# Kernel tuning notes

Hardware: AMD Instinct MI355X
Metric: run time of the kernel (lower is better)

The kernel has to match this reference:

```python
import jax, jax.numpy as jnp
import numpy as np

H = W = 224
N_LM = 8
BLOCK = 3  # patch is [x-3:x+3, y-3:y+3] -> 6x6


def _clip_coords(lm_float):
    # lm_float: [B, 16] normalized landmarks in [0,1]
    c = (lm_float * 224.0).astype(jnp.int32)
    c = jnp.where(c >= 219, 200, c)
    c = jnp.where(c <= 5, 8, c)
    return c.reshape(c.shape[0], N_LM, 2)


def _gather_patches(pred_map, coords):
    # pred_map: [B,1,H,W], coords: [B,8,2] int32 -> [B,8,36]
    B = pred_map.shape[0]
    x = coords[..., 0]  # [B,8]
    y = coords[..., 1]
    offs = jnp.arange(-BLOCK, BLOCK)  # 6 offsets
    xs = x[..., None] + offs          # [B,8,6]
    ys = y[..., None] + offs          # [B,8,6]
    b = jnp.arange(B)[:, None, None, None]
    # vectorized gather replacing the per-sample/per-landmark python loop
    patches = pred_map[b, 0, xs[:, :, :, None], ys[:, :, None, :]]  # [B,8,6,6]
    return patches.reshape(B, N_LM, (2 * BLOCK) ** 2)


def setup_inputs() -> dict:
    key = jax.random.key(0)
    ks = jax.random.split(key, 8)
    B = 512
    pred_map = jax.random.normal(ks[0], (B, 1, H, W), dtype=jnp.float32)
    Landmarks_GT = jax.random.uniform(ks[1], (B, 16), dtype=jnp.float32)
    d_in = H * W  # 50176
    s1 = 1.0 / np.sqrt(d_in)
    s2 = 1.0 / np.sqrt(512)
    s3 = 1.0 / np.sqrt(256)
    W1 = jax.random.uniform(ks[2], (d_in, 512), jnp.float32, -s1, s1)
    b1 = jax.random.uniform(ks[3], (512,), jnp.float32, -s1, s1)
    W2 = jax.random.uniform(ks[4], (512, 256), jnp.float32, -s2, s2)
    b2 = jax.random.uniform(ks[5], (256,), jnp.float32, -s2, s2)
    W3 = jax.random.uniform(ks[6], (256, 16), jnp.float32, -s3, s3)
    b3 = jax.random.uniform(ks[7], (16,), jnp.float32, -s3, s3)
    return {"pred_map": pred_map, "Landmarks_GT": Landmarks_GT,
            "W1": W1, "b1": b1, "W2": W2, "b2": b2, "W3": W3, "b3": b3}


def reference(pred_map, Landmarks_GT, W1, b1, W2, b2, W3, b3):
    B = pred_map.shape[0]
    # GT landmark patch gather
    gt_coords = _clip_coords(Landmarks_GT)
    GT_patch = _gather_patches(pred_map, gt_coords)  # [B,8,36]
    # MLP_Grah_Second on flattened pred_map
    flat = pred_map.reshape(B, -1)                   # [B,50176]
    h = jax.nn.relu(flat @ W1 + b1)
    h = jax.nn.relu(h @ W2 + b2)
    pred = jax.nn.sigmoid(h @ W3 + b3)               # [B,16]
    # predicted landmark patch gather
    pr_coords = _clip_coords(pred)
    Pred_patch = _gather_patches(pred_map, pr_coords)  # [B,8,36]
    return pred, GT_patch, Pred_patch
```

## Files before the change

### kernel.cpp

```cpp
#include <hip/hip_runtime.h>
#include <math.h>

typedef __fp16   h16x2 __attribute__((ext_vector_type(2)));
typedef _Float16 f16x8 __attribute__((ext_vector_type(8)));
typedef __attribute__((ext_vector_type(4))) float f32x4;

#define KDIM 50176
#define NDIM 512
#define MDIM 512
#define BM 256
#define BN 128
#define BK 32

__device__ __forceinline__ void split_pair(float a, float b, unsigned& hw, unsigned& lw) {
    h16x2 hp = __builtin_amdgcn_cvt_pkrtz(a, b);
    float ra = (a - (float)hp[0]) * 2048.0f;
    float rb = (b - (float)hp[1]) * 2048.0f;
    h16x2 lp = __builtin_amdgcn_cvt_pkrtz(ra, rb);
    union { h16x2 v; unsigned u; } cu;
    cu.v = hp; hw = cu.u;
    cu.v = lp; lw = cu.u;
}

__global__ __launch_bounds__(512, 2) void gemm1_mfma(
    const float* __restrict__ A,
    const float* __restrict__ W,
    float* __restrict__ part,
    int steps, int S)
{
    __shared__ float          Afs[2][256][32];
    __shared__ unsigned short Bhs[2][128][40];
    __shared__ unsigned short Bls[2][128][40];

    const int t = threadIdx.x;

    const int nwg = 8 * S;
    int l = blockIdx.x;
    if ((nwg & 7) == 0) l = (l & 7) * (nwg >> 3) + (l >> 3);
    const int z = l >> 3, bm = l & 1, bn = (l >> 1) & 3;
    const int kbase = z * steps * BK;
    const int bmBase = bm * BM;

    const int lane = t & 63, wave = t >> 6;
    const int wm = wave >> 1, wn2 = wave & 1;
    const int l15 = lane & 15, lh = lane >> 4;

    const bool isW = (t < 256);
    const int u = isW ? t : (t - 256);
    const int wkb = u & 7, wn0 = (u >> 3) * 4;

    const int aRowInWave = lane >> 3;
    const int aSwz = ((lane & 7) ^ aRowInWave) * 4;

    f32x4 acc0[4][4], acc1[4][4];
#pragma unroll
    for (int i = 0; i < 4; ++i)
#pragma unroll
        for (int j = 0; j < 4; ++j) { acc0[i][j] = (f32x4)0.f; acc1[i][j] = (f32x4)0.f; }

    float4 wreg[4];
    auto gloadW = [&](int s) {
        const float* Wb = W + (size_t)(kbase + s * BK) * NDIM + bn * BN + wn0;
#pragma unroll
        for (int i = 0; i < 4; ++i)
            wreg[i] = *(const float4*)(Wb + (size_t)(wkb * 4 + i) * NDIM);
    };
    auto gloadA = [&](int s, int buf) {
        const int k0 = kbase + s * BK;
#pragma unroll
        for (int j = 0; j < 4; ++j) {
            const int rbase = wave * 32 + j * 8;
            const float* src = A + (size_t)(bmBase + rbase + aRowInWave) * KDIM + k0 + aSwz;
            __builtin_amdgcn_global_load_lds(src, &Afs[buf][rbase][0], 16, 0, 0);
        }
    };
    auto stageW = [&](int buf, int j) {
        unsigned h01, l01, h23, l23;
        split_pair(((const float*)&wreg[0])[j] * 64.0f, ((const float*)&wreg[1])[j] * 64.0f, h01, l01);
        split_pair(((const float*)&wreg[2])[j] * 64.0f, ((const float*)&wreg[3])[j] * 64.0f, h23, l23);
        *(uint2*)&Bhs[buf][wn0 + j][wkb * 4] = make_uint2(h01, h23);
        *(uint2*)&Bls[buf][wn0 + j][wkb * 4] = make_uint2(l01, l23);
    };

    auto buildA = [&](int buf, int mf, f16x8& ahv, f16x8& alv) {
        const int m = wm * 64 + mf * 16 + l15;
        const int s0 = ((2 * lh) ^ (l15 & 7)) * 4;
        const int s1 = ((2 * lh + 1) ^ (l15 & 7)) * 4;
        float4 f0 = *(const float4*)&Afs[buf][m][s0];
        float4 f1 = *(const float4*)&Afs[buf][m][s1];
        union { unsigned uu[4]; f16x8 v; } H, L;
        split_pair(f0.x, f0.y, H.uu[0], L.uu[0]);
        split_pair(f0.z, f0.w, H.uu[1], L.uu[1]);
        split_pair(f1.x, f1.y, H.uu[2], L.uu[2]);
        split_pair(f1.z, f1.w, H.uu[3], L.uu[3]);
        ahv = H.v; alv = L.v;
    };

    if (isW) gloadW(0);
    gloadA(0, 0);
    if (isW) {
#pragma unroll
        for (int j = 0; j < 4; ++j) stageW(0, j);
    }
    __syncthreads();

    int cur = 0;
    for (int s = 0; s < steps; ++s) {
        const bool pf = (s + 1 < steps);
        if (pf) {
            if (isW) gloadW(s + 1);
            gloadA(s + 1, cur ^ 1);
        }

        f16x8 bh[4], bl[4];
#pragma unroll
        for (int nf = 0; nf < 4; ++nf) {
            bh[nf] = *(const f16x8*)&Bhs[cur][wn2 * 64 + nf * 16 + l15][lh * 8];
            bl[nf] = *(const f16x8*)&Bls[cur][wn2 * 64 + nf * 16 + l15][lh * 8];
        }

        f16x8 ah[2], al[2];
        buildA(cur, 0, ah[0], al[0]);

#pragma unroll
        for (int mf = 0; mf < 4; ++mf) {
            const int c = mf & 1, n = c ^ 1;
            if (mf < 3) buildA(cur, mf + 1, ah[n], al[n]);
            __builtin_amdgcn_s_setprio(1);
#pragma unroll
            for (int nf = 0; nf < 4; ++nf) {
                acc0[mf][nf] = __builtin_amdgcn_mfma_f32_16x16x32_f16(ah[c], bh[nf], acc0[mf][nf], 0, 0, 0);
                acc1[mf][nf] = __builtin_amdgcn_mfma_f32_16x16x32_f16(ah[c], bl[nf], acc1[mf][nf], 0, 0, 0);
                acc1[mf][nf] = __builtin_amdgcn_mfma_f32_16x16x32_f16(al[c], bh[nf], acc1[mf][nf], 0, 0, 0);
            }
            __builtin_amdgcn_s_setprio(0);
            if (pf && isW) stageW(cur ^ 1, mf);
        }
        __syncthreads();
        cur ^= 1;
    }

    const float c0 = 1.0f / 64.0f;
    const float c1 = 1.0f / 131072.0f;
    float* Cp = part + (size_t)z * (MDIM * NDIM);
    const int row0 = bmBase + wm * 64;
    const int col0 = bn * BN + wn2 * 64;
#pragma unroll
    for (int mf = 0; mf < 4; ++mf)
#pragma unroll
        for (int nf = 0; nf < 4; ++nf) {
            const int r0 = row0 + mf * 16 + lh * 4;
            const int c = col0 + nf * 16 + l15;
#pragma unroll
            for (int r = 0; r < 4; ++r)
                Cp[(size_t)(r0 + r) * NDIM + c] = acc0[mf][nf][r] * c0 + acc1[mf][nf][r] * c1;
        }
}

__global__ __launch_bounds__(256) void reduce_bias_relu(
    const float4* __restrict__ part, const float* __restrict__ b1,
    float4* __restrict__ h1, int S)
{
    int i = blockIdx.x * 256 + threadIdx.x;
    float4 s = make_float4(0.f, 0.f, 0.f, 0.f);
    for (int z = 0; z < S; ++z) {
        float4 v = part[(size_t)z * 65536 + i];
        s.x += v.x; s.y += v.y; s.z += v.z; s.w += v.w;
    }
    int nb = (i & 127) * 4;
    s.x = fmaxf(s.x + b1[nb + 0], 0.f);
    s.y = fmaxf(s.y + b1[nb + 1], 0.f);
    s.z = fmaxf(s.z + b1[nb + 2], 0.f);
    s.w = fmaxf(s.w + b1[nb + 3], 0.f);
    h1[i] = s;
}

__global__ __launch_bounds__(256) void gemm2_k(
    const float* __restrict__ h1, const float* __restrict__ W2,
    const float* __restrict__ b2, float* __restrict__ h2)
{
    int g = blockIdx.x * 256 + threadIdx.x;
    int m = g >> 8, n = g & 255;
    const float* a = h1 + (size_t)m * 512;
    float sum = 0.f;
#pragma unroll 8
    for (int k = 0; k < 512; ++k) sum = fmaf(a[k], W2[(size_t)k * 256 + n], sum);
    sum += b2[n];
    h2[g] = fmaxf(sum, 0.f);
}

__global__ __launch_bounds__(256) void gemm3_sig(
    const float* __restrict__ h2, const float* __restrict__ W3,
    const float* __restrict__ b3, float* __restrict__ pred)
{
    int g = blockIdx.x * 256 + threadIdx.x;
    int m = g >> 4, j = g & 15;
    const float* a = h2 + (size_t)m * 256;
    float sum = 0.f;
#pragma unroll 8
    for (int k = 0; k < 256; ++k) sum = fmaf(a[k], W3[(size_t)k * 16 + j], sum);
    sum += b3[j];
    pred[g] = 1.f / (1.f + expf(-sum));
}

__device__ __forceinline__ int clip_coord(float v) {
    int c = (int)(v * 224.0f);
    if (c >= 219) c = 200;
    if (c <= 5)   c = 8;
    return c;
}

__global__ void patches_k(
    const float* __restrict__ pm, const float* __restrict__ gt,
    const float* __restrict__ pred, float* __restrict__ out)
{
    const int b = blockIdx.x;
    const int t = threadIdx.x;
    const int lm = t / 36, cell = t % 36;
    const int dx = cell / 6 - 3, dy = cell % 6 - 3;
    const float* pmb = pm + (size_t)b * 50176;
    {
        int cx = clip_coord(gt[b * 16 + lm * 2 + 0]);
        int cy = clip_coord(gt[b * 16 + lm * 2 + 1]);
        out[8192 + b * 288 + t] = pmb[(cx + dx) * 224 + (cy + dy)];
    }
    {
        int cx = clip_coord(pred[b * 16 + lm * 2 + 0]);
        int cy = clip_coord(pred[b * 16 + lm * 2 + 1]);
        out[8192 + 147456 + b * 288 + t] = pmb[(cx + dx) * 224 + (cy + dy)];
    }
}

extern "C" void kernel_launch(void* const* d_in, const int* in_sizes, int n_in,
                              void* d_out, int out_size, void* d_ws, size_t ws_size,
                              hipStream_t stream)
{
    const float* pred_map = (const float*)d_in[0];
    const float* gt       = (const float*)d_in[1];
    const float* W1       = (const float*)d_in[2];
    const float* b1       = (const float*)d_in[3];
    const float* W2       = (const float*)d_in[4];
    const float* b2       = (const float*)d_in[5];
    const float* W3       = (const float*)d_in[6];
    const float* b3       = (const float*)d_in[7];
    float* out = (float*)d_out;

    float* h1   = (float*)d_ws;
    float* h2   = h1 + 262144;
    float* part = h2 + 131072;

    static const int cand[] = {32, 16, 8, 4, 2, 1};
    int S = 1;
    for (int i = 0; i < 6; ++i) {
        size_t need = (size_t)(393216 + (size_t)cand[i] * 262144) * sizeof(float);
        if (need <= ws_size) { S = cand[i]; break; }
    }
    const int steps = 1568 / S;

    hipLaunchKernelGGL(gemm1_mfma, dim3(8 * S), dim3(512), 0, stream,
                       pred_map, W1, part, steps, S);
    hipLaunchKernelGGL(reduce_bias_relu, dim3(256), dim3(256), 0, stream,
                       (const float4*)part, b1, (float4*)h1, S);
    hipLaunchKernelGGL(gemm2_k, dim3(131072 / 256), dim3(256), 0, stream, h1, W2, b2, h2);
    hipLaunchKernelGGL(gemm3_sig, dim3(8192 / 256), dim3(256), 0, stream, h2, W3, b3, out);
    hipLaunchKernelGGL(patches_k, dim3(512), dim3(288), 0, stream, pred_map, gt, out, out);
}
```

Before: 159.0 us.

## Pre-split activations into fp16 hi/lo tiles in a separate pass before GEMM1

Adds a presplit kernel that converts pred_map once into swizzled fp16 high/low tile planes in workspace, and a new GEMM1 variant that loads these pre-split tiles straight into LDS. Before, each of the four N-column workgroups repeated the split for the same A tile. The change removes that redundant ALU work from the MFMA loop. In exchange it adds an extra pass that reads A and writes A-sized data, plus a workspace requirement; the old path stays as a fallback when workspace is too small.

After: 199.6 us. 25.6% more time.

```diff
diff --git a/kernel.cpp b/kernel.cpp
--- a/kernel.cpp
+++ b/kernel.cpp
@@ -3,7 +3,7 @@
 
 typedef __fp16   h16x2 __attribute__((ext_vector_type(2)));
 typedef _Float16 f16x8 __attribute__((ext_vector_type(8)));
-typedef __attribute__((ext_vector_type(4))) float f32x4;
+typedef __attribute__((ext_vector_type(4))) float    f32x4;
 
 #define KDIM 50176
 #define NDIM 512
@@ -11,6 +11,9 @@
 #define BM 256
 #define BN 128
 #define BK 32
+#define NSTEPS 1568
+#define TILE_HALFS 16384
+#define APL_FLOATS 25690112
 
 __device__ __forceinline__ void split_pair(float a, float b, unsigned& hw, unsigned& lw) {
     h16x2 hp = __builtin_amdgcn_cvt_pkrtz(a, b);
@@ -22,18 +25,162 @@
     cu.v = lp; lw = cu.u;
 }
 
-__global__ __launch_bounds__(512, 2) void gemm1_mfma(
-    const float* __restrict__ A,
+__global__ __launch_bounds__(256) void presplit_a(
+    const float* __restrict__ A, unsigned* __restrict__ Apl)
+{
+    const int NU = 2 * NSTEPS * 256 * 4;
+    for (int u = blockIdx.x * 256 + threadIdx.x; u < NU; u += gridDim.x * 256) {
+        const int kg = u & 3;
+        const int m  = (u >> 2) & 255;
+        const int ti = u >> 10;
+        const int s  = ti % NSTEPS;
+        const int bm = ti / NSTEPS;
+        const float* src = A + (size_t)(bm * 256 + m) * KDIM + s * BK + kg * 8;
+        float4 f0 = *(const float4*)(src);
+        float4 f1 = *(const float4*)(src + 4);
+        unsigned h0, h1, h2, h3, l0, l1, l2, l3;
+        split_pair(f0.x, f0.y, h0, l0);
+        split_pair(f0.z, f0.w, h1, l1);
+        split_pair(f1.x, f1.y, h2, l2);
+        split_pair(f1.z, f1.w, h3, l3);
+        unsigned* base = Apl + (size_t)ti * (TILE_HALFS / 2) + m * 32;
+        const int hs = (kg ^ (m & 7)) * 4;
+        const int ls = ((4 | kg) ^ (m & 7)) * 4;
+        *(uint4*)(base + hs) = make_uint4(h0, h1, h2, h3);
+        *(uint4*)(base + ls) = make_uint4(l0, l1, l2, l3);
+    }
+}
+
+__global__ __launch_bounds__(512, 2) void gemm1_mfma_v2(
+    const unsigned short* __restrict__ Apl,
     const float* __restrict__ W,
-    float* __restrict__ part,
-    int steps, int S)
+    float* __restrict__ part, int steps)
+{
+    __shared__ unsigned short Apls[2][TILE_HALFS];
+    __shared__ unsigned short Bhs[2][128][40];
+    __shared__ unsigned short Bls[2][128][40];
+
+    const int t = threadIdx.x;
+    const int nwg = 8 * 32;
+    int l = blockIdx.x;
+    l = (l & 7) * (nwg >> 3) + (l >> 3);
+    const int z = l >> 3, bm = l & 1, bn = (l >> 1) & 3;
+
+    const int lane = t & 63, wave = t >> 6;
+    const int wm = wave >> 1, wn2 = wave & 1;
+    const int l15 = lane & 15, lh = lane >> 4;
+
+    const bool isW = (t < 256);
+    const int u = isW ? t : (t - 256);
+    const int wkb = u & 7, wn0 = (u >> 3) * 4;
+
+    f32x4 acc0[4][4], acc1[4][4];
+#pragma unroll
+    for (int i = 0; i < 4; ++i)
+#pragma unroll
+        for (int j = 0; j < 4; ++j) { acc0[i][j] = (f32x4)0.f; acc1[i][j] = (f32x4)0.f; }
+
+    float4 wreg[4];
+    auto gloadW = [&](int s) {
+        const float* Wb = W + (size_t)((z * steps + s) * BK) * NDIM + bn * BN + wn0;
+#pragma unroll
+        for (int i = 0; i < 4; ++i)
+            wreg[i] = *(const float4*)(Wb + (size_t)(wkb * 4 + i) * NDIM);
+    };
+    auto gloadA = [&](int s, int buf) {
+        const size_t tb = (size_t)(bm * NSTEPS + z * steps + s) * TILE_HALFS;
+#pragma unroll
+        for (int j = 0; j < 4; ++j) {
+            const int off = j * 4096 + wave * 512;
+            const unsigned short* src = Apl + tb + off + lane * 8;
+            __builtin_amdgcn_global_load_lds(src, &Apls[buf][off], 16, 0, 0);
+        }
+    };
+    auto stageW = [&](int buf, int j) {
+        unsigned h01, l01, h23, l23;
+        split_pair(((const float*)&wreg[0])[j] * 64.0f, ((const float*)&wreg[1])[j] * 64.0f, h01, l01);
+        split_pair(((const float*)&wreg[2])[j] * 64.0f, ((const float*)&wreg[3])[j] * 64.0f, h23, l23);
+        *(uint2*)&Bhs[buf][wn0 + j][wkb * 4] = make_uint2(h01, h23);
+        *(uint2*)&Bls[buf][wn0 + j][wkb * 4] = make_uint2(l01, l23);
+    };
+
+    if (isW) gloadW(0);
+    gloadA(0, 0);
+    if (isW) {
+#pragma unroll
+        for (int j = 0; j < 4; ++j) stageW(0, j);
+    }
+    __syncthreads();
+
+    int cur = 0;
+    for (int s = 0; s < steps; ++s) {
+        const bool pf = (s + 1 < steps);
+        if (pf) {
+            if (isW) gloadW(s + 1);
+            gloadA(s + 1, cur ^ 1);
+        }
+
+        f16x8 bh[4], bl[4];
+#pragma unroll
+        for (int nf = 0; nf < 4; ++nf) {
+            bh[nf] = *(const f16x8*)&Bhs[cur][wn2 * 64 + nf * 16 + l15][lh * 8];
+            bl[nf] = *(const f16x8*)&Bls[cur][wn2 * 64 + nf * 16 + l15][lh * 8];
+        }
+
+        f16x8 ah[2], al[2];
+        {
+            const int m = wm * 64 + l15;
+            ah[0] = *(const f16x8*)&Apls[cur][m * 64 + ((lh ^ (m & 7)) * 8)];
+            al[0] = *(const f16x8*)&Apls[cur][m * 64 + (((4 | lh) ^ (m & 7)) * 8)];
+        }
+#pragma unroll
+        for (int mf = 0; mf < 4; ++mf) {
+            const int c = mf & 1, n = c ^ 1;
+            if (mf < 3) {
+                const int m = wm * 64 + (mf + 1) * 16 + l15;
+                ah[n] = *(const f16x8*)&Apls[cur][m * 64 + ((lh ^ (m & 7)) * 8)];
+                al[n] = *(const f16x8*)&Apls[cur][m * 64 + (((4 | lh) ^ (m & 7)) * 8)];
+            }
+            __builtin_amdgcn_s_setprio(1);
+#pragma unroll
+            for (int nf = 0; nf < 4; ++nf) {
+                acc0[mf][nf] = __builtin_amdgcn_mfma_f32_16x16x32_f16(ah[c], bh[nf], acc0[mf][nf], 0, 0, 0);
+                acc1[mf][nf] = __builtin_amdgcn_mfma_f32_16x16x32_f16(ah[c], bl[nf], acc1[mf][nf], 0, 0, 0);
+                acc1[mf][nf] = __builtin_amdgcn_mfma_f32_16x16x32_f16(al[c], bh[nf], acc1[mf][nf], 0, 0, 0);
+            }
+            __builtin_amdgcn_s_setprio(0);
+            if (pf && isW) stageW(cur ^ 1, mf);
+        }
+        __syncthreads();
+        cur ^= 1;
+    }
+
+    const float c0 = 1.0f / 64.0f;
+    const float c1 = 1.0f / 131072.0f;
+    float* Cp = part + (size_t)z * (MDIM * NDIM);
+    const int row0 = bm * BM + wm * 64;
+    const int col0 = bn * BN + wn2 * 64;
+#pragma unroll
+    for (int mf = 0; mf < 4; ++mf)
+#pragma unroll
+        for (int nf = 0; nf < 4; ++nf) {
+            const int r0 = row0 + mf * 16 + lh * 4;
+            const int c = col0 + nf * 16 + l15;
+#pragma unroll
+            for (int r = 0; r < 4; ++r)
+                Cp[(size_t)(r0 + r) * NDIM + c] = acc0[mf][nf][r] * c0 + acc1[mf][nf][r] * c1;
+        }
+}
+
+__global__ __launch_bounds__(512, 2) void gemm1_mfma_v1(
+    const float* __restrict__ A, const float* __restrict__ W,
+    float* __restrict__ part, int steps, int S)
 {
     __shared__ float          Afs[2][256][32];
     __shared__ unsigned short Bhs[2][128][40];
     __shared__ unsigned short Bls[2][128][40];
 
     const int t = threadIdx.x;
-
     const int nwg = 8 * S;
     int l = blockIdx.x;
     if ((nwg & 7) == 0) l = (l & 7) * (nwg >> 3) + (l >> 3);
@@ -48,7 +195,6 @@
     const bool isW = (t < 256);
     const int u = isW ? t : (t - 256);
     const int wkb = u & 7, wn0 = (u >> 3) * 4;
-
     const int aRowInWave = lane >> 3;
     const int aSwz = ((lane & 7) ^ aRowInWave) * 4;
 
@@ -81,18 +227,20 @@
         *(uint2*)&Bhs[buf][wn0 + j][wkb * 4] = make_uint2(h01, h23);
         *(uint2*)&Bls[buf][wn0 + j][wkb * 4] = make_uint2(l01, l23);
     };
-
     auto buildA = [&](int buf, int mf, f16x8& ahv, f16x8& alv) {
         const int m = wm * 64 + mf * 16 + l15;
         const int s0 = ((2 * lh) ^ (l15 & 7)) * 4;
         const int s1 = ((2 * lh + 1) ^ (l15 & 7)) * 4;
         float4 f0 = *(const float4*)&Afs[buf][m][s0];
         float4 f1 = *(const float4*)&Afs[buf][m][s1];
+        unsigned h0, h1, h2, h3, l0, l1, l2, l3;
+        split_pair(f0.x, f0.y, h0, l0);
+        split_pair(f0.z, f0.w, h1, l1);
+        split_pair(f1.x, f1.y, h2, l2);
+        split_pair(f1.z, f1.w, h3, l3);
         union { unsigned uu[4]; f16x8 v; } H, L;
-        split_pair(f0.x, f0.y, H.uu[0], L.uu[0]);
-        split_pair(f0.z, f0.w, H.uu[1], L.uu[1]);
-        split_pair(f1.x, f1.y, H.uu[2], L.uu[2]);
-        split_pair(f1.z, f1.w, H.uu[3], L.uu[3]);
+        H.uu[0] = h0; H.uu[1] = h1; H.uu[2] = h2; H.uu[3] = h3;
+        L.uu[0] = l0; L.uu[1] = l1; L.uu[2] = l2; L.uu[3] = l3;
         ahv = H.v; alv = L.v;
     };
 
@@ -111,17 +259,14 @@
             if (isW) gloadW(s + 1);
             gloadA(s + 1, cur ^ 1);
         }
-
         f16x8 bh[4], bl[4];
 #pragma unroll
         for (int nf = 0; nf < 4; ++nf) {
             bh[nf] = *(const f16x8*)&Bhs[cur][wn2 * 64 + nf * 16 + l15][lh * 8];
             bl[nf] = *(const f16x8*)&Bls[cur][wn2 * 64 + nf * 16 + l15][lh * 8];
         }
-
         f16x8 ah[2], al[2];
         buildA(cur, 0, ah[0], al[0]);
-
 #pragma unroll
         for (int mf = 0; mf < 4; ++mf) {
             const int c = mf & 1, n = c ^ 1;
@@ -249,18 +394,29 @@
     float* h2   = h1 + 262144;
     float* part = h2 + 131072;
 
-    static const int cand[] = {32, 16, 8, 4, 2, 1};
-    int S = 1;
-    for (int i = 0; i < 6; ++i) {
-        size_t need = (size_t)(393216 + (size_t)cand[i] * 262144) * sizeof(float);
-        if (need <= ws_size) { S = cand[i]; break; }
-    }
-    const int steps = 1568 / S;
-
-    hipLaunchKernelGGL(gemm1_mfma, dim3(8 * S), dim3(512), 0, stream,
-                       pred_map, W1, part, steps, S);
-    hipLaunchKernelGGL(reduce_bias_relu, dim3(256), dim3(256), 0, stream,
-                       (const float4*)part, b1, (float4*)h1, S);
+    const size_t need_v2 = (size_t)(393216 + 32 * 262144 + APL_FLOATS) * 4;
+
+    if (ws_size >= need_v2) {
+        unsigned* Apl = (unsigned*)(part + 32 * 262144);
+        hipLaunchKernelGGL(presplit_a, dim3(2048), dim3(256), 0, stream, pred_map, Apl);
+        hipLaunchKernelGGL(gemm1_mfma_v2, dim3(256), dim3(512), 0, stream,
+                           (const unsigned short*)Apl, W1, part, NSTEPS / 32);
+        hipLaunchKernelGGL(reduce_bias_relu, dim3(256), dim3(256), 0, stream,
+                           (const float4*)part, b1, (float4*)h1, 32);
+    } else {
+        static const int cand[] = {32, 16, 8, 4, 2, 1};
+        int S = 1;
+        for (int i = 0; i < 6; ++i) {
+            size_t need = (size_t)(393216 + (size_t)cand[i] * 262144) * sizeof(float);
+            if (need <= ws_size) { S = cand[i]; break; }
+        }
+        const int steps = NSTEPS / S;
+        hipLaunchKernelGGL(gemm1_mfma_v1, dim3(8 * S), dim3(512), 0, stream,
+                           pred_map, W1, part, steps, S);
+        hipLaunchKernelGGL(reduce_bias_relu, dim3(256), dim3(256), 0, stream,
+                           (const float4*)part, b1, (float4*)h1, S);
+    }
+
     hipLaunchKernelGGL(gemm2_k, dim3(131072 / 256), dim3(256), 0, stream, h1, W2, b2, h2);
     hipLaunchKernelGGL(gemm3_sig, dim3(8192 / 256), dim3(256), 0, stream, h2, W3, b3, out);
     hipLaunchKernelGGL(patches_k, dim3(512), dim3(288), 0, stream, pred_map, gt, out, out);
```
